# Kernel tuning notes

Hardware: AMD Instinct MI355X
Metric: run time of the kernel (lower is better)

## Reference

```python
import jax, jax.numpy as jnp
import numpy as np

DIM = 1024
NUM_HEADS = 16
DIM_HEAD = 64
FEATURE_DIM = 64
INNER = NUM_HEADS * DIM_HEAD
EPS = 1e-6


def setup_inputs() -> dict:
    key = jax.random.key(0)
    ks = jax.random.split(key, 7)
    x = jax.random.normal(ks[0], (4, 8192, DIM), dtype=jnp.float32)
    s = 1.0 / np.sqrt(DIM)
    Wq = jax.random.normal(ks[1], (DIM, INNER), dtype=jnp.float32) * s
    Wk = jax.random.normal(ks[2], (DIM, INNER), dtype=jnp.float32) * s
    Wv = jax.random.normal(ks[3], (DIM, INNER), dtype=jnp.float32) * s
    proj = jax.random.normal(ks[4], (DIM_HEAD, FEATURE_DIM), dtype=jnp.float32) / np.sqrt(FEATURE_DIM)
    Wo = jax.random.normal(ks[5], (INNER, DIM), dtype=jnp.float32) * (1.0 / np.sqrt(INNER))
    bo = jnp.zeros((DIM,), dtype=jnp.float32)
    return {"x": x, "Wq": Wq, "Wk": Wk, "Wv": Wv, "proj": proj, "Wo": Wo, "bo": bo}


def _feature_map(t, proj):
    # t: [b, h, n, d] -> relu(t @ proj) + eps : [b, h, n, f]
    return jax.nn.relu(jnp.einsum('bhnd,df->bhnf', t, proj)) + EPS


def reference(x, Wq, Wk, Wv, proj, Wo, bo):
    b, n, _ = x.shape
    def split_heads(t):
        return t.reshape(b, n, NUM_HEADS, DIM_HEAD).transpose(0, 2, 1, 3)  # [b,h,n,d]
    q = split_heads(x @ Wq)
    k = split_heads(x @ Wk)
    v = split_heads(x @ Wv)
    qf = _feature_map(q, proj)  # [b,h,n,f]
    kf = _feature_map(k, proj)  # [b,h,n,f]
    kv = jnp.einsum('bhnf,bhnd->bhfd', kf, v)          # [b,h,f,d]
    k_sum = kf.sum(axis=-2)                             # [b,h,f]
    num = jnp.einsum('bhnf,bhfd->bhnd', qf, kv)         # [b,h,n,d]
    den = jnp.einsum('bhnf,bhf->bhn', qf, k_sum) + EPS  # [b,h,n]
    out = num / den[..., None]
    out = out.transpose(0, 2, 1, 3).reshape(b, n, INNER)
    return out @ Wo + bo
```

## Files before the change

kernel.cpp:

```cpp
#include <hip/hip_runtime.h>

typedef unsigned short u16;
typedef unsigned int u32;
typedef __attribute__((ext_vector_type(4))) float f32x4;
typedef __attribute__((ext_vector_type(4))) u16 u16x4;
typedef __attribute__((ext_vector_type(8))) u16 u16x8;
typedef __attribute__((ext_vector_type(8))) __bf16 bf16x8;

#define FLA_EPS 1e-6f

__device__ __forceinline__ u16 f2b(float f) {
  union { float f; u32 u; } v; v.f = f;
  u32 r = v.u + 0x7FFFu + ((v.u >> 16) & 1u);
  return (u16)(r >> 16);
}
__device__ __forceinline__ float b2f(u16 h) {
  union { u32 u; float f; } v; v.u = ((u32)h) << 16; return v.f;
}
__device__ __forceinline__ float bsum8(bf16x8 v) {
  union { bf16x8 b; u16x8 u; } x; x.b = v;
  float s = 0.f;
#pragma unroll
  for (int e = 0; e < 8; ++e) s += b2f(x.u[e]);
  return s;
}
__device__ __forceinline__ void g2l16(const void* g, void* l) {
  __builtin_amdgcn_global_load_lds((__attribute__((address_space(1))) void*)g,
                                   (__attribute__((address_space(3))) void*)l,
                                   16, 0, 0);
}

__global__ void __launch_bounds__(256) prep(const float* __restrict__ x,
                                            const float* __restrict__ Wq,
                                            const float* __restrict__ Wk,
                                            const float* __restrict__ Wv,
                                            const float* __restrict__ Wo,
                                            const float* __restrict__ proj,
                                            u16* __restrict__ xb,
                                            u16* __restrict__ WqkvT,
                                            u16* __restrict__ woT,
                                            float* __restrict__ zbase) {
  __shared__ __align__(16) char smem[33280];
  const int blk = blockIdx.x;
  const int t = threadIdx.x;
  if (blk < 16384) {
    size_t i = (size_t)blk * 256 + t;
    const f32x4* p = (const f32x4*)x + i * 2;
    f32x4 a = p[0], b = p[1];
    u16x8 r;
    r[0] = f2b(a[0]); r[1] = f2b(a[1]); r[2] = f2b(a[2]); r[3] = f2b(a[3]);
    r[4] = f2b(b[0]); r[5] = f2b(b[1]); r[6] = f2b(b[2]); r[7] = f2b(b[3]);
    ((u16x8*)xb)[i] = r;
  } else if (blk < 16896) {
    const int b2 = blk - 16384;
    const int kbase = (b2 & 15) * 64, h = (b2 >> 4) & 15, sel = b2 >> 8;
    float (*Wt)[65] = (float(*)[65])smem;
    float (*P)[64] = (float(*)[64])(smem + 16640);
    const float* W = sel ? Wk : Wq;
    {
      int row = t >> 2, cb = (t & 3) * 16;
#pragma unroll
      for (int i = 0; i < 4; ++i) {
        f32x4 vv = *(const f32x4*)(W + (size_t)(kbase + row) * 1024 + h * 64 + cb + i * 4);
        Wt[row][cb + i * 4 + 0] = vv[0]; Wt[row][cb + i * 4 + 1] = vv[1];
        Wt[row][cb + i * 4 + 2] = vv[2]; Wt[row][cb + i * 4 + 3] = vv[3];
        f32x4 pp = *(const f32x4*)(proj + (size_t)row * 64 + cb + i * 4);
        P[row][cb + i * 4 + 0] = pp[0]; P[row][cb + i * 4 + 1] = pp[1];
        P[row][cb + i * 4 + 2] = pp[2]; P[row][cb + i * 4 + 3] = pp[3];
      }
    }
    __syncthreads();
    const int kk = t & 63, fg = (t >> 6) * 16;
    float acc[16] = {};
    for (int d = 0; d < 64; ++d) {
      float w = Wt[kk][d];
#pragma unroll
      for (int ff = 0; ff < 16; ++ff) acc[ff] = fmaf(w, P[d][fg + ff], acc[ff]);
    }
#pragma unroll
    for (int ff = 0; ff < 16; ++ff)
      WqkvT[(size_t)(sel * 1024 + h * 64 + fg + ff) * 1024 + kbase + kk] = f2b(acc[ff]);
  } else if (blk < 17408) {
    const bool isV = blk < 17152;
    const int b3 = blk - (isV ? 16896 : 17152);
    const float* W = isV ? Wv : Wo;
    u16* Wt_out = isV ? (WqkvT + (size_t)2048 * 1024) : woT;
    float (*tile)[65] = (float(*)[65])smem;
    const int k0 = (b3 & 15) * 64, n0 = (b3 >> 4) * 64;
    const int r = t >> 4, c4 = (t & 15) * 4;
#pragma unroll
    for (int i = 0; i < 4; ++i) {
      f32x4 vv = *(const f32x4*)(W + (size_t)(k0 + r + i * 16) * 1024 + n0 + c4);
      tile[r + i * 16][c4 + 0] = vv[0];
      tile[r + i * 16][c4 + 1] = vv[1];
      tile[r + i * 16][c4 + 2] = vv[2];
      tile[r + i * 16][c4 + 3] = vv[3];
    }
    __syncthreads();
#pragma unroll
    for (int i = 0; i < 4; ++i) {
      int nrow = r + i * 16;
      u16x4 o;
#pragma unroll
      for (int j = 0; j < 4; ++j) o[j] = f2b(tile[c4 + j][nrow]);
      *(u16x4*)(Wt_out + (size_t)(n0 + nrow) * 1024 + k0 + c4) = o;
    }
  } else {
    const size_t i = (size_t)(blk - 17408) * 256 + t;
    if (i < 66560) {
      f32x4 z = {0.f, 0.f, 0.f, 0.f};
      ((f32x4*)zbase)[i] = z;
    }
  }
}

template <int NB, bool QKV>
__global__ void __launch_bounds__(512) gemm256(const u16* __restrict__ Ax,
                                               const u16* __restrict__ Bt,
                                               u16* __restrict__ qo, u16* __restrict__ ko,
                                               u16* __restrict__ vo,
                                               float* __restrict__ Cf,
                                               const float* __restrict__ bias) {
  extern __shared__ __align__(16) u16 lds[];
  const int tid = threadIdx.x;
  const int flat = blockIdx.x;
  const int xcd = flat & 7, slot = flat >> 3;
  const int pos = slot & 7, g = slot >> 3;
  const int nc = g % NB, mc = g / NB;
  const int m0 = (xcd * 16 + mc * 8 + pos) * 256;
  const int n0 = nc * 256;
  const int w = tid >> 6, l = tid & 63, quad = l >> 4, lr = l & 15;
  const int wm = w >> 2, wn = w & 3;
  u16* const A0 = lds;
  u16* const B0 = lds + 16384;
  u16* const A1 = lds + 32768;
  u16* const B1 = lds + 49152;
  const int c0 = ((quad * 16) ^ ((lr & 7) << 4)) >> 1;
  const int c1 = ((64 + quad * 16) ^ ((lr & 7) << 4)) >> 1;
  const int rst = tid >> 3;
  const int ksw8 = ((tid & 7) ^ (rst & 7)) * 8;
  const int tid8 = tid * 8;

  f32x4 acc[8][4] = {};
  bf16x8 af[4][2];
  bf16x8 bl[2][2];
  bf16x8 bh[2][2];

#define STG(SRC, ROW0, KT, DST) do {                                         \
    const u16* s_ = (SRC) + (size_t)((ROW0) + rst) * 1024 + (KT) + ksw8;     \
    g2l16(s_, (DST) + tid8);                                                 \
    g2l16(s_ + 64 * 1024, (DST) + 4096 + tid8);                              \
  } while (0)

#define RD_A(BASE, MH) do {                                                  \
    const u16* ap_ = (BASE) + wm * 8192 + (MH) * 4096;                       \
    _Pragma("unroll")                                                        \
    for (int ii = 0; ii < 4; ++ii) {                                         \
      const int ro_ = (ii * 16 + lr) * 64;                                   \
      af[ii][0] = *(const bf16x8*)(ap_ + ro_ + c0);                          \
      af[ii][1] = *(const bf16x8*)(ap_ + ro_ + c1);                          \
    } } while (0)

#define RD_B(DST2, BASE, J0) do {                                            \
    const u16* bp_ = (BASE) + (wn >> 1) * 8192 + (wn & 1) * 4096;            \
    _Pragma("unroll")                                                        \
    for (int jj = 0; jj < 2; ++jj) {                                         \
      const int ro_ = (((J0) + jj) * 16 + lr) * 64;                          \
      DST2[jj][0] = *(const bf16x8*)(bp_ + ro_ + c0);                        \
      DST2[jj][1] = *(const bf16x8*)(bp_ + ro_ + c1);                        \
    } } while (0)

#define CL(MH, BF2, NH) do {                                                 \
    __builtin_amdgcn_s_setprio(1);                                           \
    _Pragma("unroll")                                                        \
    for (int ii = 0; ii < 4; ++ii)                                           \
      _Pragma("unroll")                                                      \
      for (int jj = 0; jj < 2; ++jj)                                         \
        _Pragma("unroll")                                                    \
        for (int ks = 0; ks < 2; ++ks)                                       \
          acc[(MH) * 4 + ii][(NH) * 2 + jj] =                                \
              __builtin_amdgcn_mfma_f32_16x16x32_bf16(                       \
                  af[ii][ks], BF2[jj][ks],                                   \
                  acc[(MH) * 4 + ii][(NH) * 2 + jj], 0, 0, 0);               \
    __builtin_amdgcn_s_setprio(0);                                           \
  } while (0)

#define SB0() __builtin_amdgcn_sched_barrier(0)
#define WAIT_LGKM(N) do { asm volatile("s_waitcnt lgkmcnt(" #N ")" ::: "memory"); SB0(); } while (0)
#define WAIT_VM0()   do { asm volatile("s_waitcnt vmcnt(0)" ::: "memory"); SB0(); } while (0)
#define BARRIER()    do { asm volatile("s_barrier" ::: "memory"); SB0(); } while (0)

  STG(Ax, m0, 0, A0); STG(Ax, m0 + 128, 0, A0 + 8192);
  STG(Bt, n0, 0, B0); STG(Bt, n0 + 128, 0, B0 + 8192);
  STG(Ax, m0, 64, A1); STG(Ax, m0 + 128, 64, A1 + 8192);
  STG(Bt, n0, 64, B1); STG(Bt, n0 + 128, 64, B1 + 8192);
  asm volatile("s_waitcnt vmcnt(8)" ::: "memory");
  SB0();
  BARRIER();
  RD_B(bl, B0, 0);
  RD_A(A0, 0);
  RD_B(bh, B0, 2);
  SB0();

#pragma unroll
  for (int t = 0; t < 16; ++t) {
    u16* const Ac = (t & 1) ? A1 : A0;
    u16* const Bc = (t & 1) ? B1 : B0;
    u16* const An = (t & 1) ? A0 : A1;
    u16* const Bn = (t & 1) ? B0 : B1;
    WAIT_LGKM(4);
    CL(0, bl, 0);
    WAIT_LGKM(0);
    CL(0, bh, 1);
    SB0();
    RD_A(Ac, 1);
    WAIT_LGKM(0);
    CL(1, bl, 0);
    SB0();
    if (t < 15) {
      WAIT_VM0();
      BARRIER();
      if (t < 14) {
        STG(Ax, m0,       (t + 2) * 64, Ac);
        STG(Ax, m0 + 128, (t + 2) * 64, Ac + 8192);
        STG(Bt, n0,       (t + 2) * 64, Bc);
        STG(Bt, n0 + 128, (t + 2) * 64, Bc + 8192);
      }
      RD_B(bl, Bn, 0);
      SB0();
    }
    CL(1, bh, 1);
    SB0();
    if (t < 15) {
      RD_A(An, 0);
      RD_B(bh, Bn, 2);
      SB0();
    }
  }
#undef STG
#undef RD_A
#undef RD_B
#undef CL
#undef WAIT_LGKM
#undef WAIT_VM0
#undef BARRIER

  const int rbase = m0 + wm * 128 + quad * 4;
  if (QKV) {
    const int sel = n0 >> 10;
    if (sel == 0) {
      const int cb = (n0 & 1023) + wn * 64 + lr;
#pragma unroll
      for (int mi = 0; mi < 8; ++mi)
#pragma unroll
        for (int nj = 0; nj < 4; ++nj)
#pragma unroll
          for (int rr = 0; rr < 4; ++rr) {
            int row = rbase + mi * 16 + rr;
            float v = fmaxf(acc[mi][nj][rr], 0.0f) + FLA_EPS;
            qo[(size_t)row * 1024 + cb + nj * 16] = f2b(v);
          }
    } else {
      const bool isK = (sel == 1);
      __syncthreads();
#pragma unroll
      for (int mi = 0; mi < 8; ++mi)
#pragma unroll
        for (int nj = 0; nj < 4; ++nj) {
          const int r0 = wm * 128 + mi * 16 + quad * 4;
          const int c = wn * 64 + nj * 16 + lr;
          u16x4 pk;
#pragma unroll
          for (int rr = 0; rr < 4; ++rr) {
            float v = acc[mi][nj][rr];
            if (isK) v = fmaxf(v, 0.0f) + FLA_EPS;
            pk[rr] = f2b(v);
          }
          *(u16x4*)&lds[c * 256 + (((r0 >> 3) ^ (c & 7)) << 3) + (r0 & 7)] = pk;
        }
      __syncthreads();
      u16* dstT = isK ? ko : vo;
      const int bI = m0 >> 13, s0 = m0 & 8191;
      const size_t cb0 = ((size_t)bI << 10) + (n0 & 1023);
#pragma unroll
      for (int i = 0; i < 16; ++i) {
        const int c = w * 32 + i * 2 + (l >> 5);
        const int u = (l & 31) ^ (c & 7);
        u16x8 vv = *(const u16x8*)&lds[c * 256 + u * 8];
        *(u16x8*)(dstT + (cb0 + c) * 8192 + s0 + (l & 31) * 8) = vv;
      }
    }
  } else {
#pragma unroll
    for (int mi = 0; mi < 8; ++mi)
#pragma unroll
      for (int nj = 0; nj < 4; ++nj) {
        const int cb = n0 + wn * 64 + nj * 16 + lr;
#pragma unroll
        for (int rr = 0; rr < 4; ++rr) {
          int row = rbase + mi * 16 + rr;
          Cf[(size_t)row * 1024 + cb] = acc[mi][nj][rr] + bias[cb];
        }
      }
  }
}

__global__ void __launch_bounds__(256) kv_mfma(const u16* __restrict__ kT,
                                               const u16* __restrict__ vT,
                                               float* __restrict__ kvT,
                                               float* __restrict__ ksum) {
  __shared__ __align__(16) u16 Av[2][4096];
  __shared__ __align__(16) u16 Bk[2][4096];
  const int tid = threadIdx.x;
  const int bh = blockIdx.x, chunk = blockIdx.y;
  const size_t n0 = (size_t)chunk * 1024;
  const u16* vbp = vT + (size_t)bh * 64 * 8192;
  const u16* kbp = kT + (size_t)bh * 64 * 8192;
  const int w = tid >> 6, l = tid & 63, quad = l >> 4, lr = l & 15;
  const int wd = w >> 1, wf = w & 1;
  const int dstg = tid >> 3, kc = tid & 7;
  const int sc0 = (kc ^ (dstg & 7)) * 8;
  f32x4 acc[2][2] = {};
  float ksm[2] = {0.f, 0.f};

#define KVSTG(BUF, T) do {                                                    \
    const size_t off_ = n0 + (size_t)(T) * 64;                                \
    g2l16(vbp + (size_t)dstg * 8192 + off_ + sc0, &Av[BUF][tid8_]);           \
    g2l16(vbp + (size_t)(dstg + 32) * 8192 + off_ + sc0, &Av[BUF][2048 + tid8_]); \
    g2l16(kbp + (size_t)dstg * 8192 + off_ + sc0, &Bk[BUF][tid8_]);           \
    g2l16(kbp + (size_t)(dstg + 32) * 8192 + off_ + sc0, &Bk[BUF][2048 + tid8_]); \
  } while (0)
  const int tid8_ = tid * 8;

  KVSTG(0, 0);
  for (int t = 0; t < 16; ++t) {
    const int buf = t & 1;
    if (t < 15) {
      KVSTG(buf ^ 1, t + 1);
      asm volatile("s_waitcnt vmcnt(4)" ::: "memory");
    } else {
      asm volatile("s_waitcnt vmcnt(0)" ::: "memory");
    }
    __builtin_amdgcn_sched_barrier(0);
    __builtin_amdgcn_s_barrier();
    bf16x8 av[2][2], bk[2][2];
#pragma unroll
    for (int di = 0; di < 2; ++di)
#pragma unroll
      for (int ks = 0; ks < 2; ++ks) {
        const int d = wd * 32 + di * 16 + lr;
        av[di][ks] = *(const bf16x8*)&Av[buf][d * 64 + ((ks * 4 + quad) ^ (d & 7)) * 8];
        const int f = wf * 32 + di * 16 + lr;
        bk[di][ks] = *(const bf16x8*)&Bk[buf][f * 64 + ((ks * 4 + quad) ^ (f & 7)) * 8];
      }
    asm volatile("s_waitcnt lgkmcnt(0)" ::: "memory");
    __builtin_amdgcn_sched_barrier(0);
#pragma unroll
    for (int di = 0; di < 2; ++di)
#pragma unroll
      for (int fj = 0; fj < 2; ++fj)
#pragma unroll
        for (int ks = 0; ks < 2; ++ks)
          acc[di][fj] = __builtin_amdgcn_mfma_f32_16x16x32_bf16(
              av[di][ks], bk[fj][ks], acc[di][fj], 0, 0, 0);
    if (w < 2) {
#pragma unroll
      for (int fj = 0; fj < 2; ++fj) {
        ksm[fj] += bsum8(bk[fj][0]);
        ksm[fj] += bsum8(bk[fj][1]);
      }
    }
    __builtin_amdgcn_s_barrier();
  }
#undef KVSTG

  float* pb = kvT + (size_t)bh * 4096;
#pragma unroll
  for (int di = 0; di < 2; ++di)
#pragma unroll
    for (int fj = 0; fj < 2; ++fj)
#pragma unroll
      for (int rr = 0; rr < 4; ++rr) {
        const int d = wd * 32 + di * 16 + quad * 4 + rr;
        const int f = wf * 32 + fj * 16 + lr;
        atomicAdd(&pb[d * 64 + f], acc[di][fj][rr]);
      }
  if (w < 2) {
#pragma unroll
    for (int fj = 0; fj < 2; ++fj) {
      float s = ksm[fj];
      s += __shfl_xor(s, 16, 64);
      s += __shfl_xor(s, 32, 64);
      if (l < 16)
        atomicAdd(&ksum[(size_t)bh * 64 + wf * 32 + fj * 16 + l], s);
    }
  }
}

__global__ void __launch_bounds__(256) num_den(const u16* __restrict__ qf,
                                               const float* __restrict__ kvT,
                                               const float* __restrict__ ksum,
                                               u16* __restrict__ outI) {
  __shared__ __align__(16) u16 As[128 * 64];
  __shared__ __align__(16) u16 Bs[64 * 64];
  __shared__ float ksum_s[64];
  __shared__ float den_s[128];
  const int t = threadIdx.x;
  const size_t tok0 = (size_t)blockIdx.x * 128;
  const int h = blockIdx.y;
  const int bh = (blockIdx.x >> 6) * 16 + h;
  const int w = t >> 6, l = t & 63, quad = l >> 4, lr = l & 15;
  const int trow = t >> 3, tcol = (t & 7) * 8;
#pragma unroll
  for (int i = 0; i < 4; ++i) {
    int r = i * 32 + trow;
    g2l16(qf + (tok0 + r) * 1024 + h * 64 + tcol, &As[r * 64 + tcol]);
  }
  {
    const float* kvb = kvT + (size_t)bh * 4096;
    int d = t >> 2, cb = (t & 3) * 16;
    u16x8 o0, o1;
#pragma unroll
    for (int q4 = 0; q4 < 2; ++q4) {
      f32x4 vv = *(const f32x4*)(kvb + d * 64 + cb + q4 * 4);
      o0[q4 * 4 + 0] = f2b(vv[0]); o0[q4 * 4 + 1] = f2b(vv[1]);
      o0[q4 * 4 + 2] = f2b(vv[2]); o0[q4 * 4 + 3] = f2b(vv[3]);
    }
#pragma unroll
    for (int q4 = 0; q4 < 2; ++q4) {
      f32x4 vv = *(const f32x4*)(kvb + d * 64 + cb + 8 + q4 * 4);
      o1[q4 * 4 + 0] = f2b(vv[0]); o1[q4 * 4 + 1] = f2b(vv[1]);
      o1[q4 * 4 + 2] = f2b(vv[2]); o1[q4 * 4 + 3] = f2b(vv[3]);
    }
    *(u16x8*)&Bs[d * 64 + cb] = o0;
    *(u16x8*)&Bs[d * 64 + cb + 8] = o1;
  }
  if (t < 64) ksum_s[t] = ksum[(size_t)bh * 64 + t];
  __syncthreads();
  if (t < 128) {
    float d = FLA_EPS;
#pragma unroll
    for (int jj = 0; jj < 64; ++jj) {
      int f = (t + jj) & 63;
      d += b2f(As[t * 64 + f]) * ksum_s[f];
    }
    den_s[t] = d;
  }
  __syncthreads();
  f32x4 acc[2][4] = {};
  const int wrow = w * 32;
#pragma unroll
  for (int ks = 0; ks < 2; ++ks) {
    bf16x8 af[2], bfr[4];
#pragma unroll
    for (int i = 0; i < 2; ++i)
      af[i] = *(const bf16x8*)&As[(wrow + i * 16 + lr) * 64 + ks * 32 + quad * 8];
#pragma unroll
    for (int j = 0; j < 4; ++j)
      bfr[j] = *(const bf16x8*)&Bs[(j * 16 + lr) * 64 + ks * 32 + quad * 8];
#pragma unroll
    for (int i = 0; i < 2; ++i)
#pragma unroll
      for (int j = 0; j < 4; ++j)
        acc[i][j] = __builtin_amdgcn_mfma_f32_16x16x32_bf16(af[i], bfr[j], acc[i][j], 0, 0, 0);
  }
#pragma unroll
  for (int i = 0; i < 2; ++i)
#pragma unroll
    for (int j = 0; j < 4; ++j)
#pragma unroll
      for (int rr = 0; rr < 4; ++rr) {
        int rloc = wrow + i * 16 + quad * 4 + rr;
        float v = acc[i][j][rr] / den_s[rloc];
        outI[(tok0 + rloc) * 1024 + h * 64 + j * 16 + lr] = f2b(v);
      }
}

extern "C" void kernel_launch(void* const* d_in, const int* in_sizes, int n_in,
                              void* d_out, int out_size, void* d_ws, size_t ws_size,
                              hipStream_t stream) {
  const float* x    = (const float*)d_in[0];
  const float* Wq   = (const float*)d_in[1];
  const float* Wk   = (const float*)d_in[2];
  const float* Wv   = (const float*)d_in[3];
  const float* proj = (const float*)d_in[4];
  const float* Wo   = (const float*)d_in[5];
  const float* bo   = (const float*)d_in[6];
  float* out = (float*)d_out;

  char* ws = (char*)d_ws;
  const size_t SZ = 1ull << 26;
  u16* xb     = (u16*)(ws + 0);
  u16* qb     = (u16*)(ws + SZ);
  u16* kb     = (u16*)(ws + 2 * SZ);
  u16* vb     = (u16*)(ws + 3 * SZ);
  u16* WqkvT  = (u16*)(ws + 4 * SZ);
  u16* woT    = (u16*)(ws + 4 * SZ + 0x600000);
  float* kvT    = (float*)(ws + 4 * SZ + 0x800000);
  float* ksum   = (float*)(ws + 4 * SZ + 0x800000 + 0x100000);

  static int attr_done = 0;
  if (!attr_done) {
    (void)hipFuncSetAttribute((const void*)gemm256<12, true>,
                              hipFuncAttributeMaxDynamicSharedMemorySize, 131072);
    (void)hipFuncSetAttribute((const void*)gemm256<4, false>,
                              hipFuncAttributeMaxDynamicSharedMemorySize, 131072);
    attr_done = 1;
  }

  prep<<<17668, 256, 0, stream>>>(x, Wq, Wk, Wv, Wo, proj, xb, WqkvT, woT, kvT);
  gemm256<12, true><<<1536, 512, 131072, stream>>>(xb, WqkvT, qb, kb, vb, nullptr, nullptr);
  kv_mfma<<<dim3(64, 8), 256, 0, stream>>>(kb, vb, kvT, ksum);
  num_den<<<dim3(256, 16), 256, 0, stream>>>(qb, kvT, ksum, xb);
  gemm256<4, false><<<512, 512, 131072, stream>>>(xb, woT, nullptr, nullptr, nullptr, out, bo);
}
```

Before: 579.1 us.

## Switch GEMM to single-buffered static LDS and split transpose epilogue in halves

```diff
diff --git a/kernel.cpp b/kernel.cpp
--- a/kernel.cpp
+++ b/kernel.cpp
@@ -121,7 +121,7 @@
                                                u16* __restrict__ vo,
                                                float* __restrict__ Cf,
                                                const float* __restrict__ bias) {
-  extern __shared__ __align__(16) u16 lds[];
+  __shared__ __align__(16) u16 lds[32768];
   const int tid = threadIdx.x;
   const int flat = blockIdx.x;
   const int xcd = flat & 7, slot = flat >> 3;
@@ -131,10 +131,8 @@
   const int n0 = nc * 256;
   const int w = tid >> 6, l = tid & 63, quad = l >> 4, lr = l & 15;
   const int wm = w >> 2, wn = w & 3;
-  u16* const A0 = lds;
-  u16* const B0 = lds + 16384;
-  u16* const A1 = lds + 32768;
-  u16* const B1 = lds + 49152;
+  u16* const As = lds;
+  u16* const Bs = lds + 16384;
   const int c0 = ((quad * 16) ^ ((lr & 7) << 4)) >> 1;
   const int c1 = ((64 + quad * 16) ^ ((lr & 7) << 4)) >> 1;
   const int rst = tid >> 3;
@@ -190,52 +188,34 @@
 #define WAIT_VM0()   do { asm volatile("s_waitcnt vmcnt(0)" ::: "memory"); SB0(); } while (0)
 #define BARRIER()    do { asm volatile("s_barrier" ::: "memory"); SB0(); } while (0)
 
-  STG(Ax, m0, 0, A0); STG(Ax, m0 + 128, 0, A0 + 8192);
-  STG(Bt, n0, 0, B0); STG(Bt, n0 + 128, 0, B0 + 8192);
-  STG(Ax, m0, 64, A1); STG(Ax, m0 + 128, 64, A1 + 8192);
-  STG(Bt, n0, 64, B1); STG(Bt, n0 + 128, 64, B1 + 8192);
-  asm volatile("s_waitcnt vmcnt(8)" ::: "memory");
-  SB0();
-  BARRIER();
-  RD_B(bl, B0, 0);
-  RD_A(A0, 0);
-  RD_B(bh, B0, 2);
-  SB0();
-
-#pragma unroll
+  STG(Ax, m0, 0, As); STG(Ax, m0 + 128, 0, As + 8192);
+  STG(Bt, n0, 0, Bs); STG(Bt, n0 + 128, 0, Bs + 8192);
+
   for (int t = 0; t < 16; ++t) {
-    u16* const Ac = (t & 1) ? A1 : A0;
-    u16* const Bc = (t & 1) ? B1 : B0;
-    u16* const An = (t & 1) ? A0 : A1;
-    u16* const Bn = (t & 1) ? B0 : B1;
+    WAIT_VM0();
+    BARRIER();
+    RD_B(bl, Bs, 0);
+    RD_A(As, 0);
+    RD_B(bh, Bs, 2);
+    SB0();
     WAIT_LGKM(4);
     CL(0, bl, 0);
     WAIT_LGKM(0);
     CL(0, bh, 1);
     SB0();
-    RD_A(Ac, 1);
+    RD_A(As, 1);
     WAIT_LGKM(0);
     CL(1, bl, 0);
     SB0();
+    BARRIER();
     if (t < 15) {
-      WAIT_VM0();
-      BARRIER();
-      if (t < 14) {
-        STG(Ax, m0,       (t + 2) * 64, Ac);
-        STG(Ax, m0 + 128, (t + 2) * 64, Ac + 8192);
-        STG(Bt, n0,       (t + 2) * 64, Bc);
-        STG(Bt, n0 + 128, (t + 2) * 64, Bc + 8192);
-      }
-      RD_B(bl, Bn, 0);
-      SB0();
+      STG(Ax, m0,       (t + 1) * 64, As);
+      STG(Ax, m0 + 128, (t + 1) * 64, As + 8192);
+      STG(Bt, n0,       (t + 1) * 64, Bs);
+      STG(Bt, n0 + 128, (t + 1) * 64, Bs + 8192);
     }
     CL(1, bh, 1);
     SB0();
-    if (t < 15) {
-      RD_A(An, 0);
-      RD_B(bh, Bn, 2);
-      SB0();
-    }
   }
 #undef STG
 #undef RD_A
@@ -262,32 +242,37 @@
           }
     } else {
       const bool isK = (sel == 1);
-      __syncthreads();
-#pragma unroll
-      for (int mi = 0; mi < 8; ++mi)
-#pragma unroll
-        for (int nj = 0; nj < 4; ++nj) {
-          const int r0 = wm * 128 + mi * 16 + quad * 4;
-          const int c = wn * 64 + nj * 16 + lr;
-          u16x4 pk;
-#pragma unroll
-          for (int rr = 0; rr < 4; ++rr) {
-            float v = acc[mi][nj][rr];
-            if (isK) v = fmaxf(v, 0.0f) + FLA_EPS;
-            pk[rr] = f2b(v);
-          }
-          *(u16x4*)&lds[c * 256 + (((r0 >> 3) ^ (c & 7)) << 3) + (r0 & 7)] = pk;
-        }
-      __syncthreads();
       u16* dstT = isK ? ko : vo;
       const int bI = m0 >> 13, s0 = m0 & 8191;
       const size_t cb0 = ((size_t)bI << 10) + (n0 & 1023);
 #pragma unroll
-      for (int i = 0; i < 16; ++i) {
-        const int c = w * 32 + i * 2 + (l >> 5);
-        const int u = (l & 31) ^ (c & 7);
-        u16x8 vv = *(const u16x8*)&lds[c * 256 + u * 8];
-        *(u16x8*)(dstT + (cb0 + c) * 8192 + s0 + (l & 31) * 8) = vv;
+      for (int p = 0; p < 2; ++p) {
+        __syncthreads();
+        if ((wn >> 1) == p) {
+#pragma unroll
+          for (int mi = 0; mi < 8; ++mi)
+#pragma unroll
+            for (int nj = 0; nj < 4; ++nj) {
+              const int r0 = wm * 128 + mi * 16 + quad * 4;
+              const int c = (wn & 1) * 64 + nj * 16 + lr;
+              u16x4 pk;
+#pragma unroll
+              for (int rr = 0; rr < 4; ++rr) {
+                float v = acc[mi][nj][rr];
+                if (isK) v = fmaxf(v, 0.0f) + FLA_EPS;
+                pk[rr] = f2b(v);
+              }
+              *(u16x4*)&lds[c * 256 + (((r0 >> 3) ^ (c & 7)) << 3) + (r0 & 7)] = pk;
+            }
+        }
+        __syncthreads();
+#pragma unroll
+        for (int i = 0; i < 8; ++i) {
+          const int c = w * 16 + i * 2 + (l >> 5);
+          const int u = (l & 31) ^ (c & 7);
+          u16x8 vv = *(const u16x8*)&lds[c * 256 + u * 8];
+          *(u16x8*)(dstT + (cb0 + p * 128 + c) * 8192 + s0 + (l & 31) * 8) = vv;
+        }
       }
     }
   } else {
@@ -499,18 +484,9 @@
   float* kvT    = (float*)(ws + 4 * SZ + 0x800000);
   float* ksum   = (float*)(ws + 4 * SZ + 0x800000 + 0x100000);
 
-  static int attr_done = 0;
-  if (!attr_done) {
-    (void)hipFuncSetAttribute((const void*)gemm256<12, true>,
-                              hipFuncAttributeMaxDynamicSharedMemorySize, 131072);
-    (void)hipFuncSetAttribute((const void*)gemm256<4, false>,
-                              hipFuncAttributeMaxDynamicSharedMemorySize, 131072);
-    attr_done = 1;
-  }
-
   prep<<<17668, 256, 0, stream>>>(x, Wq, Wk, Wv, Wo, proj, xb, WqkvT, woT, kvT);
-  gemm256<12, true><<<1536, 512, 131072, stream>>>(xb, WqkvT, qb, kb, vb, nullptr, nullptr);
+  gemm256<12, true><<<1536, 512, 0, stream>>>(xb, WqkvT, qb, kb, vb, nullptr, nullptr);
   kv_mfma<<<dim3(64, 8), 256, 0, stream>>>(kb, vb, kvT, ksum);
   num_den<<<dim3(256, 16), 256, 0, stream>>>(qb, kvT, ksum, xb);
-  gemm256<4, false><<<512, 512, 131072, stream>>>(xb, woT, nullptr, nullptr, nullptr, out, bo);
-}
+  gemm256<4, false><<<512, 512, 0, stream>>>(xb, woT, nullptr, nullptr, nullptr, out, bo);
+}
```

New measurement: 645.1 us. 11.4% more time.
